# Kernel tuning notes

Measured on AMD Instinct MI355X. Metric: run time of the kernel, lower is better.

## Reference

```python
import jax, jax.numpy as jnp
import numpy as np

B, S, E, H = 4, 2048, 512, 8
HD = E // H
MLP = 4 * E
EPS = 1e-5


def layer_norm(x, g, b):
    mu = jnp.mean(x, axis=-1, keepdims=True)
    var = jnp.var(x, axis=-1, keepdims=True)
    return (x - mu) * jax.lax.rsqrt(var + EPS) * g + b


def setup_inputs() -> dict:
    key = jax.random.key(0)
    ks = jax.random.split(key, 8)
    s = 0.02
    return {
        "query": jax.random.normal(ks[0], (B, S, E), dtype=jnp.float32),
        "ln1_g": jnp.ones((E,), jnp.float32),
        "ln1_b": jnp.zeros((E,), jnp.float32),
        "in_proj_w": jax.random.normal(ks[1], (3 * E, E), jnp.float32) * s,
        "in_proj_b": jnp.zeros((3 * E,), jnp.float32),
        "out_w": jax.random.normal(ks[2], (E, E), jnp.float32) * s,
        "out_b": jnp.zeros((E,), jnp.float32),
        "ln2_g": jnp.ones((E,), jnp.float32),
        "ln2_b": jnp.zeros((E,), jnp.float32),
        "w1": jax.random.normal(ks[3], (MLP, E), jnp.float32) * s,
        "b1": jnp.zeros((MLP,), jnp.float32),
        "w2": jax.random.normal(ks[4], (E, MLP), jnp.float32) * s,
        "b2": jnp.zeros((E,), jnp.float32),
    }


def reference(query, ln1_g, ln1_b, in_proj_w, in_proj_b, out_w, out_b,
              ln2_g, ln2_b, w1, b1, w2, b2):
    # Pre-LN self-attention; key=value=normed query (is_cross_attention=False).
    xq = layer_norm(query, ln1_g, ln1_b)  # [B,S,E]
    qkv = xq @ in_proj_w.T + in_proj_b    # [B,S,3E]
    q, k, v = jnp.split(qkv, 3, axis=-1)
    q = q.reshape(B, S, H, HD)
    k = k.reshape(B, S, H, HD)
    v = v.reshape(B, S, H, HD)
    scale = 1.0 / jnp.sqrt(jnp.asarray(HD, q.dtype))
    scores = jnp.einsum("bqhd,bkhd->bhqk", q, k) * scale  # [B,H,S,S]
    probs = jax.nn.softmax(scores, axis=-1)
    ctx = jnp.einsum("bhqk,bkhd->bqhd", probs, v).reshape(B, S, E)
    attn_out = ctx @ out_w.T + out_b
    # need_weights=True, average_attn_weights default True -> mean over heads
    attn_weight = jnp.mean(probs, axis=1)  # [B,S,S]
    x = query + attn_out  # LayerScale is Identity (init_layer_scale_ratio=None)
    h = layer_norm(x, ln2_g, ln2_b)
    mlp = jax.nn.gelu(h @ w1.T + b1, approximate=False) @ w2.T + b2
    x = x + mlp
    return (x, attn_weight)
```

## Files before the change

### kernel.cpp

```cpp
#include <hip/hip_runtime.h>
#include <math.h>

#define B_ 4
#define S_ 2048
#define E_ 512
#define H_ 8
#define MLP_ 2048

typedef unsigned short u16;
typedef __attribute__((ext_vector_type(8))) short bf16x8;
typedef __attribute__((ext_vector_type(4))) float f32x4;

#define MFMA(a, b, c) __builtin_amdgcn_mfma_f32_16x16x32_bf16(a, b, c, 0, 0, 0)
#define QSCALE 0.18033688011112042f
#define hexp2(x) __builtin_amdgcn_exp2f(x)

__device__ __forceinline__ u16 f2bf(float f) {
  unsigned u = __builtin_bit_cast(unsigned, f);
  unsigned r = (u + 0x7FFFu + ((u >> 16) & 1u)) >> 16;
  return (u16)r;
}
__device__ __forceinline__ unsigned cvtpk(float a, float b) {
  unsigned r;
  asm("v_cvt_pk_bf16_f32 %0, %1, %2" : "=v"(r) : "v"(a), "v"(b));
  return r;
}
__device__ __forceinline__ void gload_lds16(const void* g, void* l) {
  __builtin_amdgcn_global_load_lds(
      (const __attribute__((address_space(1))) unsigned int*)g,
      (__attribute__((address_space(3))) unsigned int*)l, 16, 0, 0);
}
__device__ __forceinline__ float gelu_fast(float v) {
  float u = v * (0.7978845608028654f + 0.03567740813636141f * v * v);
  float e = hexp2(u * -2.885390081777927f);
  return v * __builtin_amdgcn_rcpf(1.0f + e);
}

__global__ __launch_bounds__(256) void prep_k(const float* __restrict__ s0, u16* __restrict__ d0,
                                              const float* __restrict__ s1, u16* __restrict__ d1,
                                              const float* __restrict__ s2, u16* __restrict__ d2,
                                              const float* __restrict__ s3, u16* __restrict__ d3,
                                              const float* __restrict__ x, const float* __restrict__ g,
                                              const float* __restrict__ bta, u16* __restrict__ out) {
  int bid = blockIdx.x;
  if (bid < 3072) {
    const float* s; u16* d; int i;
    if (bid < 768)       { s = s0; d = d0; i = bid * 256 + threadIdx.x; }
    else if (bid < 1024) { s = s1; d = d1; i = (bid - 768) * 256 + threadIdx.x; }
    else if (bid < 2048) { s = s2; d = d2; i = (bid - 1024) * 256 + threadIdx.x; }
    else                 { s = s3; d = d3; i = (bid - 2048) * 256 + threadIdx.x; }
    float4 v = reinterpret_cast<const float4*>(s)[i];
    union { u16 u[4]; uint2 q; } p;
    p.u[0] = f2bf(v.x); p.u[1] = f2bf(v.y); p.u[2] = f2bf(v.z); p.u[3] = f2bf(v.w);
    reinterpret_cast<uint2*>(d)[i] = p.q;
    return;
  }
  int row = (bid - 3072) * 4 + (threadIdx.x >> 6);
  int l = threadIdx.x & 63;
  const float4* xr = reinterpret_cast<const float4*>(x + (size_t)row * 512);
  float4 a = xr[l], c = xr[l + 64];
  float s = a.x + a.y + a.z + a.w + c.x + c.y + c.z + c.w;
  float q = a.x*a.x + a.y*a.y + a.z*a.z + a.w*a.w + c.x*c.x + c.y*c.y + c.z*c.z + c.w*c.w;
  #pragma unroll
  for (int off = 32; off >= 1; off >>= 1) { s += __shfl_xor(s, off); q += __shfl_xor(q, off); }
  float mu = s * (1.0f / 512.0f);
  float var = q * (1.0f / 512.0f) - mu * mu;
  float rs = rsqrtf(var + 1e-5f);
  const float4* gv = reinterpret_cast<const float4*>(g);
  const float4* bv = reinterpret_cast<const float4*>(bta);
  #pragma unroll
  for (int half = 0; half < 2; ++half) {
    int idx = l + half * 64;
    float4 gg = gv[idx], bb = bv[idx];
    float4 vv = (half == 0) ? a : c;
    union { u16 u[4]; uint2 q2; } p;
    p.u[0] = f2bf((vv.x - mu) * rs * gg.x + bb.x);
    p.u[1] = f2bf((vv.y - mu) * rs * gg.y + bb.y);
    p.u[2] = f2bf((vv.z - mu) * rs * gg.z + bb.z);
    p.u[3] = f2bf((vv.w - mu) * rs * gg.w + bb.w);
    *reinterpret_cast<uint2*>(out + (size_t)row * 512 + idx * 4) = p.q2;
  }
}

__global__ __launch_bounds__(256) void ln_k(const float* __restrict__ x, const float* __restrict__ g,
                                            const float* __restrict__ bta, u16* __restrict__ out) {
  int row = blockIdx.x * 4 + (threadIdx.x >> 6);
  int l = threadIdx.x & 63;
  const float4* xr = reinterpret_cast<const float4*>(x + (size_t)row * 512);
  float4 a = xr[l], c = xr[l + 64];
  float s = a.x + a.y + a.z + a.w + c.x + c.y + c.z + c.w;
  float q = a.x*a.x + a.y*a.y + a.z*a.z + a.w*a.w + c.x*c.x + c.y*c.y + c.z*c.z + c.w*c.w;
  #pragma unroll
  for (int off = 32; off >= 1; off >>= 1) { s += __shfl_xor(s, off); q += __shfl_xor(q, off); }
  float mu = s * (1.0f / 512.0f);
  float var = q * (1.0f / 512.0f) - mu * mu;
  float rs = rsqrtf(var + 1e-5f);
  const float4* gv = reinterpret_cast<const float4*>(g);
  const float4* bv = reinterpret_cast<const float4*>(bta);
  #pragma unroll
  for (int half = 0; half < 2; ++half) {
    int idx = l + half * 64;
    float4 gg = gv[idx], bb = bv[idx];
    float4 vv = (half == 0) ? a : c;
    union { u16 u[4]; uint2 q2; } p;
    p.u[0] = f2bf((vv.x - mu) * rs * gg.x + bb.x);
    p.u[1] = f2bf((vv.y - mu) * rs * gg.y + bb.y);
    p.u[2] = f2bf((vv.z - mu) * rs * gg.z + bb.z);
    p.u[3] = f2bf((vv.w - mu) * rs * gg.w + bb.w);
    *reinterpret_cast<uint2*>(out + (size_t)row * 512 + idx * 4) = p.q2;
  }
}

template <int EPI>
__global__ __launch_bounds__(256) void gemm_nt(const u16* __restrict__ A, const u16* __restrict__ Bw,
                                               const float* __restrict__ bias,
                                               const float* __restrict__ resid,
                                               void* __restrict__ Cout, u16* __restrict__ vTout,
                                               int M, int N, int K) {
  __shared__ u16 lA[128 * 64];
  __shared__ u16 lB[128 * 64];
  int t = threadIdx.x, w = t >> 6, l = t & 63;
  int orig = blockIdx.y * gridDim.x + blockIdx.x;
  int cpx = (gridDim.x * gridDim.y) >> 3;
  int swz = (orig & 7) * cpx + (orig >> 3);
  int m0 = (swz / gridDim.x) * 128, n0 = (swz % gridDim.x) * 128;
  int wr = w >> 1, wc = w & 1;
  int rl = l & 15, hi = l >> 4;
  f32x4 zero = {0.f, 0.f, 0.f, 0.f};
  f32x4 acc[4][4];
  #pragma unroll
  for (int mi = 0; mi < 4; ++mi)
    #pragma unroll
    for (int ni = 0; ni < 4; ++ni) acc[mi][ni] = zero;

  for (int k0 = 0; k0 < K; k0 += 64) {
    #pragma unroll
    for (int it = 0; it < 4; ++it) {
      int cid = it * 256 + t;
      int row = cid >> 3, g = cid & 7;
      int gs = (g ^ (row & 7)) * 8;
      gload_lds16(A + (size_t)(m0 + row) * K + k0 + gs, lA + (size_t)cid * 8);
      gload_lds16(Bw + (size_t)(n0 + row) * K + k0 + gs, lB + (size_t)cid * 8);
    }
    __syncthreads();
    #pragma unroll
    for (int kk = 0; kk < 2; ++kk) {
      bf16x8 af[4], bfr[4];
      #pragma unroll
      for (int mi = 0; mi < 4; ++mi) {
        int row = wr * 64 + mi * 16 + rl;
        af[mi] = *reinterpret_cast<const bf16x8*>(&lA[row * 64 + (((kk * 4 + hi) ^ (row & 7)) * 8)]);
      }
      #pragma unroll
      for (int ni = 0; ni < 4; ++ni) {
        int row = wc * 64 + ni * 16 + rl;
        bfr[ni] = *reinterpret_cast<const bf16x8*>(&lB[row * 64 + (((kk * 4 + hi) ^ (row & 7)) * 8)]);
      }
      #pragma unroll
      for (int mi = 0; mi < 4; ++mi)
        #pragma unroll
        for (int ni = 0; ni < 4; ++ni) acc[mi][ni] = MFMA(af[mi], bfr[ni], acc[mi][ni]);
    }
    __syncthreads();
  }
  int rg = hi * 4;
  #pragma unroll
  for (int mi = 0; mi < 4; ++mi) {
    #pragma unroll
    for (int ni = 0; ni < 4; ++ni) {
      int gn = n0 + wc * 64 + ni * 16 + rl;
      float bvv = bias[gn];
      #pragma unroll
      for (int r = 0; r < 4; ++r) {
        int gm = m0 + wr * 64 + mi * 16 + rg + r;
        size_t off = (size_t)gm * N + gn;
        float v = acc[mi][ni][r] + bvv;
        if (EPI == 0) {
          ((u16*)Cout)[off] = f2bf(v);
        } else if (EPI == 1) {
          ((float*)Cout)[off] = v + resid[off];
        } else if (EPI == 2) {
          ((u16*)Cout)[off] = f2bf(gelu_fast(v));
        } else {
          int key = gm & 2047, bb = gm >> 11;
          if (gn < 512) {
            ((u16*)Cout)[off] = f2bf(v * QSCALE);
          } else if (gn < 1024) {
            ((u16*)Cout)[off] = f2bf(v);
          } else {
            int d = gn - 1024;
            int kin = key & 63;
            int pc = (key & ~63) + ((kin & 15) * 4 + (kin >> 4));
            vTout[((size_t)(bb * 8 + (d >> 6)) * 64 + (d & 63)) * 2048 + pc] = f2bf(v);
          }
        }
      }
    }
  }
}

__global__ __launch_bounds__(256) void gemm_n64_k(const u16* __restrict__ A, const u16* __restrict__ Bw,
                                                  const float* __restrict__ bias,
                                                  const float* __restrict__ resid,
                                                  float* __restrict__ Cout,
                                                  int M, int N, int K) {
  __shared__ u16 lA[2][128 * 64];
  __shared__ u16 lB[2][64 * 64];
  int t = threadIdx.x, w = t >> 6, l = t & 63;
  int orig = blockIdx.y * gridDim.x + blockIdx.x;
  int cpx = (gridDim.x * gridDim.y) >> 3;
  int swz = (orig & 7) * cpx + (orig >> 3);
  int m0 = (swz / gridDim.x) * 128, n0 = (swz % gridDim.x) * 64;
  int wr = w >> 1, wc = w & 1;
  int rl = l & 15, hi = l >> 4;
  f32x4 zero = {0.f, 0.f, 0.f, 0.f};
  f32x4 acc[4][2];
  #pragma unroll
  for (int mi = 0; mi < 4; ++mi)
    #pragma unroll
    for (int ni = 0; ni < 2; ++ni) acc[mi][ni] = zero;

  #pragma unroll
  for (int it = 0; it < 4; ++it) {
    int cid = it * 256 + t;
    int row = cid >> 3, g = cid & 7;
    int gs = (g ^ (row & 7)) * 8;
    gload_lds16(A + (size_t)(m0 + row) * K + gs, &lA[0][(size_t)cid * 8]);
  }
  #pragma unroll
  for (int it = 0; it < 2; ++it) {
    int cid = it * 256 + t;
    int row = cid >> 3, g = cid & 7;
    int gs = (g ^ (row & 7)) * 8;
    gload_lds16(Bw + (size_t)(n0 + row) * K + gs, &lB[0][(size_t)cid * 8]);
  }
  __syncthreads();
  int nk = K >> 6;
  for (int kt = 0; kt < nk; ++kt) {
    int cur = kt & 1;
    if (kt + 1 < nk) {
      int k0 = (kt + 1) << 6;
      #pragma unroll
      for (int it = 0; it < 4; ++it) {
        int cid = it * 256 + t;
        int row = cid >> 3, g = cid & 7;
        int gs = (g ^ (row & 7)) * 8;
        gload_lds16(A + (size_t)(m0 + row) * K + k0 + gs, &lA[cur ^ 1][(size_t)cid * 8]);
      }
      #pragma unroll
      for (int it = 0; it < 2; ++it) {
        int cid = it * 256 + t;
        int row = cid >> 3, g = cid & 7;
        int gs = (g ^ (row & 7)) * 8;
        gload_lds16(Bw + (size_t)(n0 + row) * K + k0 + gs, &lB[cur ^ 1][(size_t)cid * 8]);
      }
    }
    #pragma unroll
    for (int kk = 0; kk < 2; ++kk) {
      bf16x8 af[4], bfr[2];
      #pragma unroll
      for (int mi = 0; mi < 4; ++mi) {
        int row = wr * 64 + mi * 16 + rl;
        af[mi] = *reinterpret_cast<const bf16x8*>(&lA[cur][row * 64 + (((kk * 4 + hi) ^ (row & 7)) * 8)]);
      }
      #pragma unroll
      for (int ni = 0; ni < 2; ++ni) {
        int row = wc * 32 + ni * 16 + rl;
        bfr[ni] = *reinterpret_cast<const bf16x8*>(&lB[cur][row * 64 + (((kk * 4 + hi) ^ (row & 7)) * 8)]);
      }
      #pragma unroll
      for (int mi = 0; mi < 4; ++mi)
        #pragma unroll
        for (int ni = 0; ni < 2; ++ni) acc[mi][ni] = MFMA(af[mi], bfr[ni], acc[mi][ni]);
    }
    __syncthreads();
  }
  int rg = hi * 4;
  #pragma unroll
  for (int mi = 0; mi < 4; ++mi) {
    #pragma unroll
    for (int ni = 0; ni < 2; ++ni) {
      int gn = n0 + wc * 32 + ni * 16 + rl;
      float bvv = bias[gn];
      #pragma unroll
      for (int r = 0; r < 4; ++r) {
        int gm = m0 + wr * 64 + mi * 16 + rg + r;
        size_t off = (size_t)gm * N + gn;
        Cout[off] = acc[mi][ni][r] + bvv + resid[off];
      }
    }
  }
}

__global__ __launch_bounds__(512) void attn_fctx7_k(const u16* __restrict__ qkv,
                                                    const u16* __restrict__ vT,
                                                    float* __restrict__ rinv,
                                                    u16* __restrict__ ctx) {
  __shared__ u16 kbuf[2][64 * 64];
  __shared__ u16 vbuf[2][64 * 64];
  __shared__ u16 pl[8][16][72];
  int t = threadIdx.x, w = t >> 6, l = t & 63;
  int n = blockIdx.x + 16 * (blockIdx.y + 8 * blockIdx.z);
  int slot = n >> 3;
  int g = (n & 7) * 4 + (slot >> 4);
  int qb = slot & 15;
  int h = g >> 2, b = g & 3;
  int qt = qb * 128 + w * 16;
  int rl = l & 15, hi = l >> 4;
  f32x4 zero = {0.f, 0.f, 0.f, 0.f};
  bf16x8 q0 = *reinterpret_cast<const bf16x8*>(
      qkv + (size_t)(b * S_ + qt + rl) * 1536 + h * 64 + hi * 8);
  bf16x8 q1 = *reinterpret_cast<const bf16x8*>(
      qkv + (size_t)(b * S_ + qt + rl) * 1536 + h * 64 + 32 + hi * 8);
  f32x4 acc[4];
  float lsp[4];
  #pragma unroll
  for (int dc = 0; dc < 4; ++dc) acc[dc] = zero;
  #pragma unroll
  for (int r = 0; r < 4; ++r) lsp[r] = 0.f;
  {
    int r = t >> 3, gp = t & 7, gl = gp ^ (r & 7);
    gload_lds16(qkv + (size_t)(b * S_ + r) * 1536 + 512 + h * 64 + gl * 8, &kbuf[0][t * 8]);
    gload_lds16(vT + ((size_t)(b * H_ + h) * 64 + r) * 2048 + gl * 8, &vbuf[0][t * 8]);
  }
  __syncthreads();
  for (int kt = 0; kt < 32; ++kt) {
    int cur = kt & 1;
    if (kt + 1 < 32) {
      int r = t >> 3, gp = t & 7, gl = gp ^ (r & 7);
      gload_lds16(qkv + (size_t)(b * S_ + (kt + 1) * 64 + r) * 1536 + 512 + h * 64 + gl * 8,
                  &kbuf[cur ^ 1][t * 8]);
      gload_lds16(vT + ((size_t)(b * H_ + h) * 64 + r) * 2048 + (kt + 1) * 64 + gl * 8,
                  &vbuf[cur ^ 1][t * 8]);
    }
    const u16* kb = kbuf[cur];
    const u16* vb = vbuf[cur];
    f32x4 s[4];
    __builtin_amdgcn_s_setprio(1);
    #pragma unroll
    for (int j = 0; j < 4; ++j) {
      int row = j * 16 + rl;
      bf16x8 k0 = *reinterpret_cast<const bf16x8*>(kb + row * 64 + ((hi ^ (row & 7)) * 8));
      bf16x8 k1 = *reinterpret_cast<const bf16x8*>(kb + row * 64 + (((hi + 4) ^ (row & 7)) * 8));
      s[j] = MFMA(q0, k0, zero);
      s[j] = MFMA(q1, k1, s[j]);
    }
    __builtin_amdgcn_s_setprio(0);
    #pragma unroll
    for (int r = 0; r < 4; ++r) {
      float p0 = hexp2(s[0][r]);
      float p1 = hexp2(s[1][r]);
      float p2 = hexp2(s[2][r]);
      float p3 = hexp2(s[3][r]);
      lsp[r] += (p0 + p1) + (p2 + p3);
      uint2 pk;
      pk.x = cvtpk(p0, p1);
      pk.y = cvtpk(p2, p3);
      *reinterpret_cast<uint2*>(&pl[w][hi * 4 + r][rl * 4]) = pk;
    }
    bf16x8 pf0 = *reinterpret_cast<const bf16x8*>(&pl[w][rl][hi * 8]);
    bf16x8 pf1 = *reinterpret_cast<const bf16x8*>(&pl[w][rl][32 + hi * 8]);
    __builtin_amdgcn_s_setprio(1);
    #pragma unroll
    for (int dc = 0; dc < 4; ++dc) {
      int row = dc * 16 + rl;
      bf16x8 v0 = *reinterpret_cast<const bf16x8*>(vb + row * 64 + ((hi ^ (row & 7)) * 8));
      bf16x8 v1 = *reinterpret_cast<const bf16x8*>(vb + row * 64 + (((hi + 4) ^ (row & 7)) * 8));
      acc[dc] = MFMA(pf0, v0, acc[dc]);
      acc[dc] = MFMA(pf1, v1, acc[dc]);
    }
    __builtin_amdgcn_s_setprio(0);
    __syncthreads();
  }
  #pragma unroll
  for (int r = 0; r < 4; ++r) {
    float v = lsp[r];
    #pragma unroll
    for (int off = 8; off >= 1; off >>= 1) v += __shfl_xor(v, off, 16);
    lsp[r] = v;
  }
  #pragma unroll
  for (int dc = 0; dc < 4; ++dc)
    #pragma unroll
    for (int r = 0; r < 4; ++r)
      ctx[(size_t)(b * S_ + qt + hi * 4 + r) * 512 + h * 64 + dc * 16 + rl] =
          f2bf(acc[dc][r] / lsp[r]);
  if (rl == 0) {
    #pragma unroll
    for (int r = 0; r < 4; ++r)
      rinv[(size_t)(b * H_ + h) * S_ + qt + hi * 4 + r] = 0.125f / lsp[r];
  }
}

__global__ __launch_bounds__(256) void attn_mean10_k(const u16* __restrict__ qkv,
                                                     const float* __restrict__ rinv,
                                                     float* __restrict__ attn) {
  __shared__ u16 lQ[2][128 * 64];
  __shared__ u16 lK[2][128 * 64];
  int t = threadIdx.x, w = t >> 6, l = t & 63;
  int kt = blockIdx.x, qt = blockIdx.y, b = blockIdx.z;
  int wr = w >> 1, wc = w & 1;
  int rl = l & 15, hi = l >> 4;
  f32x4 zero = {0.f, 0.f, 0.f, 0.f};
  f32x4 acc[4][4];
  #pragma unroll
  for (int mi = 0; mi < 4; ++mi)
    #pragma unroll
    for (int ni = 0; ni < 4; ++ni) acc[mi][ni] = zero;

  const u16* qbase = qkv + (size_t)(b * S_ + qt * 128) * 1536;
  const u16* kbase = qkv + (size_t)(b * S_ + kt * 128) * 1536 + 512;
  #pragma unroll
  for (int it = 0; it < 4; ++it) {
    int cid = it * 256 + t;
    int row = cid >> 3, g = cid & 7;
    int gs = (g ^ (row & 7)) * 8;
    gload_lds16(qbase + (size_t)row * 1536 + gs, &lQ[0][cid * 8]);
    gload_lds16(kbase + (size_t)row * 1536 + gs, &lK[0][cid * 8]);
  }
  __syncthreads();
  for (int h = 0; h < 8; ++h) {
    int cur = h & 1;
    if (h + 1 < 8) {
      #pragma unroll
      for (int it = 0; it < 4; ++it) {
        int cid = it * 256 + t;
        int row = cid >> 3, g = cid & 7;
        int gs = (g ^ (row & 7)) * 8;
        gload_lds16(qbase + (size_t)row * 1536 + (h + 1) * 64 + gs, &lQ[cur ^ 1][cid * 8]);
        gload_lds16(kbase + (size_t)row * 1536 + (h + 1) * 64 + gs, &lK[cur ^ 1][cid * 8]);
      }
    }
    float4 rv[4];
    #pragma unroll
    for (int mi = 0; mi < 4; ++mi)
      rv[mi] = *reinterpret_cast<const float4*>(
          rinv + (size_t)(b * H_ + h) * S_ + qt * 128 + wr * 64 + mi * 16 + hi * 4);
    f32x4 s[4][4];
    __builtin_amdgcn_s_setprio(1);
    #pragma unroll
    for (int kk = 0; kk < 2; ++kk) {
      bf16x8 af[4], bfr[4];
      #pragma unroll
      for (int mi = 0; mi < 4; ++mi) {
        int row = wr * 64 + mi * 16 + rl;
        af[mi] = *reinterpret_cast<const bf16x8*>(&lQ[cur][row * 64 + (((kk * 4 + hi) ^ (row & 7)) * 8)]);
      }
      #pragma unroll
      for (int ni = 0; ni < 4; ++ni) {
        int row = wc * 64 + ni * 16 + rl;
        bfr[ni] = *reinterpret_cast<const bf16x8*>(&lK[cur][row * 64 + (((kk * 4 + hi) ^ (row & 7)) * 8)]);
      }
      #pragma unroll
      for (int mi = 0; mi < 4; ++mi)
        #pragma unroll
        for (int ni = 0; ni < 4; ++ni)
          s[mi][ni] = (kk == 0) ? MFMA(af[mi], bfr[ni], zero) : MFMA(af[mi], bfr[ni], s[mi][ni]);
    }
    __builtin_amdgcn_s_setprio(0);
    #pragma unroll
    for (int mi = 0; mi < 4; ++mi) {
      float rva[4] = {rv[mi].x, rv[mi].y, rv[mi].z, rv[mi].w};
      #pragma unroll
      for (int ni = 0; ni < 4; ++ni)
        #pragma unroll
        for (int r = 0; r < 4; ++r)
          acc[mi][ni][r] += hexp2(s[mi][ni][r]) * rva[r];
    }
    __syncthreads();
  }
  #pragma unroll
  for (int mi = 0; mi < 4; ++mi)
    #pragma unroll
    for (int r = 0; r < 4; ++r) {
      size_t rowoff = (size_t)(b * S_ + qt * 128 + wr * 64 + mi * 16 + hi * 4 + r) * 2048 +
                      kt * 128 + wc * 64 + rl;
      #pragma unroll
      for (int ni = 0; ni < 4; ++ni)
        attn[rowoff + ni * 16] = acc[mi][ni][r];
    }
}

extern "C" void kernel_launch(void* const* d_in, const int* in_sizes, int n_in,
                              void* d_out, int out_size, void* d_ws, size_t ws_size,
                              hipStream_t stream) {
  const float* query     = (const float*)d_in[0];
  const float* ln1_g     = (const float*)d_in[1];
  const float* ln1_b     = (const float*)d_in[2];
  const float* in_proj_w = (const float*)d_in[3];
  const float* in_proj_b = (const float*)d_in[4];
  const float* out_w     = (const float*)d_in[5];
  const float* out_b     = (const float*)d_in[6];
  const float* ln2_g     = (const float*)d_in[7];
  const float* ln2_b     = (const float*)d_in[8];
  const float* w1        = (const float*)d_in[9];
  const float* b1        = (const float*)d_in[10];
  const float* w2        = (const float*)d_in[11];
  const float* b2        = (const float*)d_in[12];

  u16* ws = (u16*)d_ws;
  u16* wq_bf = ws;
  u16* wo_bf = wq_bf + 1536 * 512;
  u16* w1_bf = wo_bf + 512 * 512;
  u16* w2_bf = w1_bf + 2048 * 512;
  u16* xq_bf = w2_bf + 512 * 2048;
  u16* qkv_bf = xq_bf + 8192 * 512;
  u16* ctx_bf = qkv_bf + 8192 * 1536;
  u16* h_bf   = ctx_bf + 8192 * 512;
  u16* mh_bf  = h_bf + 8192 * 512;
  float* rinv = (float*)(mh_bf + 8192 * 2048);
  u16* vT = mh_bf;

  float* xout = (float*)d_out;
  float* attn = xout + (size_t)8192 * 512;

  prep_k<<<5120, 256, 0, stream>>>(in_proj_w, wq_bf, out_w, wo_bf, w1, w1_bf, w2, w2_bf,
                                   query, ln1_g, ln1_b, xq_bf);

  gemm_nt<3><<<dim3(12, 64), 256, 0, stream>>>(xq_bf, wq_bf, in_proj_b, nullptr, qkv_bf, vT, 8192, 1536, 512);

  attn_fctx7_k<<<dim3(16, 8, 4), 512, 0, stream>>>(qkv_bf, vT, rinv, ctx_bf);

  attn_mean10_k<<<dim3(16, 16, 4), 256, 0, stream>>>(qkv_bf, rinv, attn);

  gemm_n64_k<<<dim3(8, 64), 256, 0, stream>>>(ctx_bf, wo_bf, out_b, query, xout, 8192, 512, 512);

  ln_k<<<2048, 256, 0, stream>>>(xout, ln2_g, ln2_b, h_bf);

  gemm_nt<2><<<dim3(16, 64), 256, 0, stream>>>(h_bf, w1_bf, b1, nullptr, mh_bf, nullptr, 8192, 2048, 512);

  gemm_n64_k<<<dim3(8, 64), 256, 0, stream>>>(mh_bf, w2_bf, b2, xout, xout, 8192, 512, 2048);
}
```

Before: 199.8 us.

## Compute transposed scores so probabilities feed PV MFMA directly from registers

Swaps the MFMA operand order for QK^T so each lane holds score values along the key dimension, which lets the exponentiated probabilities be packed straight into the A operand of the PV MFMA. This removes the per-wave LDS scratch buffer and its write/read round-trip each key tile. To match the new register layout, the V-transpose permutation in the QKV GEMM epilogue changes. Row sums are now reduced with a different shuffle pattern. It relies on getting the permutation exactly right across two kernels.

```diff
diff --git a/kernel.cpp b/kernel.cpp
--- a/kernel.cpp
+++ b/kernel.cpp
@@ -190,7 +190,8 @@
           } else {
             int d = gn - 1024;
             int kin = key & 63;
-            int pc = (key & ~63) + ((kin & 15) * 4 + (kin >> 4));
+            int pc = (key & ~63) +
+                     (((kin >> 5) << 5) | (((kin >> 2) & 3) << 3) | (((kin >> 4) & 1) << 2) | (kin & 3));
             vTout[((size_t)(bb * 8 + (d >> 6)) * 64 + (d & 63)) * 2048 + pc] = f2bf(v);
           }
         }
@@ -292,13 +293,12 @@
   }
 }
 
-__global__ __launch_bounds__(512) void attn_fctx7_k(const u16* __restrict__ qkv,
+__global__ __launch_bounds__(512) void attn_fctx8_k(const u16* __restrict__ qkv,
                                                     const u16* __restrict__ vT,
                                                     float* __restrict__ rinv,
                                                     u16* __restrict__ ctx) {
   __shared__ u16 kbuf[2][64 * 64];
   __shared__ u16 vbuf[2][64 * 64];
-  __shared__ u16 pl[8][16][72];
   int t = threadIdx.x, w = t >> 6, l = t & 63;
   int n = blockIdx.x + 16 * (blockIdx.y + 8 * blockIdx.z);
   int slot = n >> 3;
@@ -313,11 +313,9 @@
   bf16x8 q1 = *reinterpret_cast<const bf16x8*>(
       qkv + (size_t)(b * S_ + qt + rl) * 1536 + h * 64 + 32 + hi * 8);
   f32x4 acc[4];
-  float lsp[4];
+  float lspq = 0.f;
   #pragma unroll
   for (int dc = 0; dc < 4; ++dc) acc[dc] = zero;
-  #pragma unroll
-  for (int r = 0; r < 4; ++r) lsp[r] = 0.f;
   {
     int r = t >> 3, gp = t & 7, gl = gp ^ (r & 7);
     gload_lds16(qkv + (size_t)(b * S_ + r) * 1536 + 512 + h * 64 + gl * 8, &kbuf[0][t * 8]);
@@ -342,54 +340,48 @@
       int row = j * 16 + rl;
       bf16x8 k0 = *reinterpret_cast<const bf16x8*>(kb + row * 64 + ((hi ^ (row & 7)) * 8));
       bf16x8 k1 = *reinterpret_cast<const bf16x8*>(kb + row * 64 + (((hi + 4) ^ (row & 7)) * 8));
-      s[j] = MFMA(q0, k0, zero);
-      s[j] = MFMA(q1, k1, s[j]);
+      s[j] = MFMA(k0, q0, zero);
+      s[j] = MFMA(k1, q1, s[j]);
     }
     __builtin_amdgcn_s_setprio(0);
-    #pragma unroll
-    for (int r = 0; r < 4; ++r) {
-      float p0 = hexp2(s[0][r]);
-      float p1 = hexp2(s[1][r]);
-      float p2 = hexp2(s[2][r]);
-      float p3 = hexp2(s[3][r]);
-      lsp[r] += (p0 + p1) + (p2 + p3);
-      uint2 pk;
-      pk.x = cvtpk(p0, p1);
-      pk.y = cvtpk(p2, p3);
-      *reinterpret_cast<uint2*>(&pl[w][hi * 4 + r][rl * 4]) = pk;
-    }
-    bf16x8 pf0 = *reinterpret_cast<const bf16x8*>(&pl[w][rl][hi * 8]);
-    bf16x8 pf1 = *reinterpret_cast<const bf16x8*>(&pl[w][rl][32 + hi * 8]);
+    float p[4][4];
+    #pragma unroll
+    for (int j = 0; j < 4; ++j)
+      #pragma unroll
+      for (int r = 0; r < 4; ++r) {
+        p[j][r] = hexp2(s[j][r]);
+        lspq += p[j][r];
+      }
+    union { unsigned u[4]; bf16x8 v; } pa0, pa1;
+    pa0.u[0] = cvtpk(p[0][0], p[0][1]); pa0.u[1] = cvtpk(p[0][2], p[0][3]);
+    pa0.u[2] = cvtpk(p[1][0], p[1][1]); pa0.u[3] = cvtpk(p[1][2], p[1][3]);
+    pa1.u[0] = cvtpk(p[2][0], p[2][1]); pa1.u[1] = cvtpk(p[2][2], p[2][3]);
+    pa1.u[2] = cvtpk(p[3][0], p[3][1]); pa1.u[3] = cvtpk(p[3][2], p[3][3]);
     __builtin_amdgcn_s_setprio(1);
     #pragma unroll
     for (int dc = 0; dc < 4; ++dc) {
       int row = dc * 16 + rl;
       bf16x8 v0 = *reinterpret_cast<const bf16x8*>(vb + row * 64 + ((hi ^ (row & 7)) * 8));
       bf16x8 v1 = *reinterpret_cast<const bf16x8*>(vb + row * 64 + (((hi + 4) ^ (row & 7)) * 8));
-      acc[dc] = MFMA(pf0, v0, acc[dc]);
-      acc[dc] = MFMA(pf1, v1, acc[dc]);
+      acc[dc] = MFMA(pa0.v, v0, acc[dc]);
+      acc[dc] = MFMA(pa1.v, v1, acc[dc]);
     }
     __builtin_amdgcn_s_setprio(0);
     __syncthreads();
   }
-  #pragma unroll
-  for (int r = 0; r < 4; ++r) {
-    float v = lsp[r];
-    #pragma unroll
-    for (int off = 8; off >= 1; off >>= 1) v += __shfl_xor(v, off, 16);
-    lsp[r] = v;
-  }
+  lspq += __shfl_xor(lspq, 16);
+  lspq += __shfl_xor(lspq, 32);
+  float lr[4];
+  #pragma unroll
+  for (int r = 0; r < 4; ++r) lr[r] = __shfl(lspq, hi * 4 + r);
   #pragma unroll
   for (int dc = 0; dc < 4; ++dc)
     #pragma unroll
     for (int r = 0; r < 4; ++r)
       ctx[(size_t)(b * S_ + qt + hi * 4 + r) * 512 + h * 64 + dc * 16 + rl] =
-          f2bf(acc[dc][r] / lsp[r]);
-  if (rl == 0) {
-    #pragma unroll
-    for (int r = 0; r < 4; ++r)
-      rinv[(size_t)(b * H_ + h) * S_ + qt + hi * 4 + r] = 0.125f / lsp[r];
-  }
+          f2bf(acc[dc][r] / lr[r]);
+  if (l < 16)
+    rinv[(size_t)(b * H_ + h) * S_ + qt + rl] = 0.125f / lspq;
 }
 
 __global__ __launch_bounds__(256) void attn_mean10_k(const u16* __restrict__ qkv,
@@ -519,7 +511,7 @@
 
   gemm_nt<3><<<dim3(12, 64), 256, 0, stream>>>(xq_bf, wq_bf, in_proj_b, nullptr, qkv_bf, vT, 8192, 1536, 512);
 
-  attn_fctx7_k<<<dim3(16, 8, 4), 512, 0, stream>>>(qkv_bf, vT, rinv, ctx_bf);
+  attn_fctx8_k<<<dim3(16, 8, 4), 512, 0, stream>>>(qkv_bf, vT, rinv, ctx_bf);
 
   attn_mean10_k<<<dim3(16, 16, 4), 256, 0, stream>>>(qkv_bf, rinv, attn);
 
```

Result: no change. 196.0 us, median of 2 (-1.9%).
